# Kernel optimization log

Measured on AMD Instinct MI355X. Metric: run time of the kernel, lower is better.

## Reference

```python
import jax, jax.numpy as jnp
import numpy as np

B, N, IN, H, L, C = 2048, 100, 64, 256, 3, 3
NEG_SLOPE = 0.2


def setup_inputs() -> dict:
    key = jax.random.key(0)
    ks = jax.random.split(key, 11)
    s = lambda k, sh: jax.random.normal(k, sh, dtype=jnp.float32) * 0.05
    return {
        'x': jax.random.normal(ks[0], (B, N, IN), dtype=jnp.float32),
        'W_exp': s(ks[1], (IN, H)), 'b_exp': s(ks[2], (H,)),
        'W_l': s(ks[3], (L, H, H)), 'b_l': s(ks[4], (L, H)),
        'W_r': s(ks[5], (L, H, H)), 'b_r': s(ks[6], (L, H)),
        'att': s(ks[7], (L, H)), 'bias': s(ks[8], (L, H)),
        'W_fc': s(ks[9], (H, C)), 'b_fc': s(ks[10], (C,)),
    }


def _make_pe(n, d):
    pos = jnp.arange(n, dtype=jnp.float32)[:, None]
    div = jnp.exp(jnp.arange(0, d, 2, dtype=jnp.float32) * (-jnp.log(jnp.float32(10000.0)) / d))
    pe = jnp.zeros((n, d), dtype=jnp.float32)
    pe = pe.at[:, 0::2].set(jnp.sin(pos * div))
    pe = pe.at[:, 1::2].set(jnp.cos(pos * div))
    return pe


def _edges(n):
    # bidirectional chain + self loops (GATv2Conv add_self_loops=True)
    src = np.concatenate([np.arange(n - 1), np.arange(1, n), np.arange(n)])
    dst = np.concatenate([np.arange(1, n), np.arange(n - 1), np.arange(n)])
    return jnp.asarray(src), jnp.asarray(dst)


def _gatv2_conv(x, src, dst, Wl, bl, Wr, br, a, b, n):
    # x: [B,N,H]; PyG GATv2Conv, heads=1, share_weights=False
    xl = x @ Wl + bl                      # source transform [B,N,H]
    xr = x @ Wr + br                      # target transform [B,N,H]
    m = jax.nn.leaky_relu(xl[:, src] + xr[:, dst], NEG_SLOPE)   # [B,E,H]
    logits = jnp.einsum('beh,h->be', m, a)                      # [B,E]
    seg_max = jax.vmap(lambda l: jax.ops.segment_max(l, dst, num_segments=n))(logits)
    ex = jnp.exp(logits - seg_max[:, dst])
    denom = jax.vmap(lambda e: jax.ops.segment_sum(e, dst, num_segments=n))(ex)
    alpha = ex / denom[:, dst]                                  # [B,E]
    msgs = alpha[:, :, None] * xl[:, src]                       # [B,E,H]
    out = jax.vmap(lambda mm: jax.ops.segment_sum(mm, dst, num_segments=n))(msgs)
    return out + b


def reference(x, W_exp, b_exp, W_l, b_l, W_r, b_r, att, bias, W_fc, b_fc):
    n = x.shape[1]
    src, dst = _edges(n)
    x0 = x @ W_exp + b_exp + _make_pe(n, W_exp.shape[1])   # expander + positional encoding
    # Faithful to original: the loop feeds batch.x (= x0) into every conv layer,
    # so the output of the loop is the LAST conv applied to x0.
    h = x0
    for l in range(W_l.shape[0]):
        h = _gatv2_conv(x0, src, dst, W_l[l], b_l[l], W_r[l], b_r[l], att[l], bias[l], n)
    pooled = h.sum(axis=1)                                 # global_add_pool -> [B,H]
    return pooled @ W_fc + b_fc                            # [B,num_classes]
```

## Files before the change

kernel.cpp:

```cpp
#include <hip/hip_runtime.h>
#include <hip/hip_bf16.h>
#include <hip/hip_fp16.h>

#define BB 2048
#define NN 100
#define INF_ 64
#define HH 256
#define CC 3
#define HP 136

typedef __attribute__((ext_vector_type(8))) _Float16 h8v;
typedef __attribute__((ext_vector_type(2))) _Float16 h2v;
typedef __attribute__((ext_vector_type(2))) __fp16   g2v;
typedef __attribute__((ext_vector_type(4))) float f4v;

static __device__ __forceinline__ unsigned int pkh(float lo, float hi) {
    union { g2v g; unsigned int u; } c;
    c.g = __builtin_amdgcn_cvt_pkrtz(lo, hi);
    return c.u;
}

__global__ __launch_bounds__(256) void precompute_k(
    const float* __restrict__ W_exp, const float* __restrict__ b_exp,
    const float* __restrict__ W_l, const float* __restrict__ b_l,
    const float* __restrict__ W_r, const float* __restrict__ b_r,
    float* __restrict__ Wcomb, float* __restrict__ cadd)
{
    int r = blockIdx.x;
    int z = blockIdx.y;
    int t = threadIdx.x;
    const float* Wg = (z ? W_r : W_l) + 2 * HH * HH;
    const float* bg = (z ? b_r : b_l) + 2 * HH;

    __shared__ float sa[HH];
    float a;
    if (r < INF_) {
        a = W_exp[r * HH + t];
    } else {
        int n = r - INF_;
        float div = expf((float)(t & 254) * (-0.03597789207803f));
        float ang = (float)n * div;
        a = b_exp[t] + ((t & 1) ? cosf(ang) : sinf(ang));
    }
    sa[t] = a;
    __syncthreads();

    float acc = 0.f;
    #pragma unroll 8
    for (int h = 0; h < HH; ++h)
        acc += sa[h] * Wg[h * HH + t];

    if (r < INF_) Wcomb[(z * INF_ + r) * HH + t] = acc;
    else          cadd[(z * NN + (r - INF_)) * HH + t] = acc + bg[t];
}

#define N_WF 32768
#define N_CF4 14336

__global__ __launch_bounds__(256) void rearrange_k(
    const float* __restrict__ Wcomb, const float* __restrict__ cadd,
    unsigned short* __restrict__ WF, float* __restrict__ CFf)
{
    int i = blockIdx.x * 256 + threadIdx.x;
    if (i < N_WF) {
        int j = i & 7, lane = (i >> 3) & 63, ks = (i >> 9) & 1;
        int nt = (i >> 10) & 15, z = (i >> 14) & 1;
        int k = ks * 32 + 4 * (lane >> 4) + (j & 3) + 16 * (j >> 2);
        int n = nt * 16 + (lane & 15);
        __half h = __float2half(Wcomb[(z * INF_ + k) * HH + n]);
        WF[i] = __half_as_ushort(h);
    } else if (i < N_WF + N_CF4) {
        int i2 = i - N_WF;
        int lane = i2 & 63, nt = (i2 >> 6) & 15;
        int zm = i2 >> 10;
        int mt = zm % 7, z = zm / 7;
        int node = mt * 16 + (lane & 15);
        int feat = nt * 16 + (lane >> 4) * 4;
        float4 v = {0.f, 0.f, 0.f, 0.f};
        if (node < NN)
            v = *(const float4*)&cadd[(z * NN + node) * HH + feat];
        *(float4*)&CFf[(size_t)i2 * 4] = v;
    }
}

__global__ __launch_bounds__(512, 4) void fused_k(
    const float* __restrict__ x,
    const unsigned short* __restrict__ WF, const float* __restrict__ CFf,
    const float* __restrict__ Wcomb, const float* __restrict__ cadd,
    const float* __restrict__ att, const float* __restrict__ bias,
    const float* __restrict__ Wfc, const float* __restrict__ bfc,
    float* __restrict__ out)
{
    __shared__ unsigned short sxl[NN * HP];
    __shared__ unsigned short sxr[NN * HP];
    __shared__ unsigned short sxs[896 * 8];
    __shared__ unsigned int satt2[HH / 2];

    int b = blockIdx.x, t = threadIdx.x;
    int wave = t >> 6, lane = t & 63, g = lane >> 4, li = lane & 15;

    if (t < HH / 2) satt2[t] = pkh(att[2 * HH + 2 * t], att[2 * HH + 2 * t + 1]);

    const float* xb = x + (size_t)b * (NN * INF_);
    for (int s = t; s < 896; s += 512) {
        int sl = s & 63, ks = (s >> 6) & 1, mt = s >> 7;
        int m = mt * 16 + (sl & 15), gg = sl >> 4;
        union { h8v v; unsigned int u[4]; } a;
        if (m < NN) {
            float4 u = *(const float4*)&xb[m * INF_ + ks * 32 + 4 * gg];
            float4 v = *(const float4*)&xb[m * INF_ + ks * 32 + 16 + 4 * gg];
            a.u[0] = pkh(u.x, u.y);
            a.u[1] = pkh(u.z, u.w);
            a.u[2] = pkh(v.x, v.y);
            a.u[3] = pkh(v.z, v.w);
        } else {
            a.u[0] = a.u[1] = a.u[2] = a.u[3] = 0u;
        }
        *(h8v*)&sxs[s * 8] = a.v;
    }

    int q8 = t >> 3, c8 = (t & 7) * 8;
    int eBL[5], eBR[5];
    bool eva[5];
    float pv[5], pa[5];
    #pragma unroll
    for (int i = 0; i < 5; ++i) {
        int e = q8 + 64 * i;
        bool inr = (e < 300);
        int es = inr ? (e / 3) : 0;
        int ed = es + (e - 3 * es) - 1;
        bool v = inr && ed >= 0 && ed < NN;
        eva[i] = v;
        int dd = v ? ed : 0;
        eBL[i] = 2 * (es * HP + c8);
        eBR[i] = 2 * (dd * HP + c8);
        pv[i] = 0.f; pa[i] = 0.f;
    }

    int z = wave >> 2;
    int w4 = wave & 3;
    __syncthreads();

    const h8v* WFp = (const h8v*)WF;
    const f4v* CF4 = (const f4v*)CFf;
    const h8v* sp  = (const h8v*)sxs;

    #pragma unroll
    for (int h = 0; h < 2; ++h) {
        int nt0 = h * 8 + w4 * 2;
        h8v w00 = WFp[((z * 16 + nt0) * 2 + 0) * 64 + lane];
        h8v w01 = WFp[((z * 16 + nt0) * 2 + 1) * 64 + lane];
        h8v w10 = WFp[((z * 16 + nt0 + 1) * 2 + 0) * 64 + lane];
        h8v w11 = WFp[((z * 16 + nt0 + 1) * 2 + 1) * 64 + lane];
        unsigned short* dstp = z ? sxr : sxl;
        int colbase = w4 * 32 + g * 4;
        #pragma unroll
        for (int mt = 0; mt < 7; ++mt) {
            h8v a0 = sp[mt * 128 + lane];
            h8v a1 = sp[mt * 128 + 64 + lane];
            int node = mt * 16 + li;
            bool wr = (mt < 6 || li < 4);
            int el = node * HP + colbase;

            f4v c0 = CF4[((z * 7 + mt) * 16 + nt0) * 64 + lane];
            c0 = __builtin_amdgcn_mfma_f32_16x16x32_f16(w00, a0, c0, 0, 0, 0);
            c0 = __builtin_amdgcn_mfma_f32_16x16x32_f16(w01, a1, c0, 0, 0, 0);
            if (wr) {
                uint2 v0 = { pkh(c0[0], c0[1]), pkh(c0[2], c0[3]) };
                *(uint2*)&dstp[el] = v0;
            }
            f4v c1 = CF4[((z * 7 + mt) * 16 + nt0 + 1) * 64 + lane];
            c1 = __builtin_amdgcn_mfma_f32_16x16x32_f16(w10, a0, c1, 0, 0, 0);
            c1 = __builtin_amdgcn_mfma_f32_16x16x32_f16(w11, a1, c1, 0, 0, 0);
            if (wr) {
                uint2 v1 = { pkh(c1[0], c1[1]), pkh(c1[2], c1[3]) };
                *(uint2*)&dstp[el + 16] = v1;
            }
        }
        __syncthreads();

        #pragma unroll
        for (int cc = 0; cc < 2; ++cc) {
            uint4 atv = *(const uint4*)&satt2[h * 64 + cc * 32 + (t & 7) * 4];
            int cb = cc * 128;
            #pragma unroll
            for (int i = 0; i < 5; ++i) {
                if (eva[i]) {
                    uint4 ua = *(const uint4*)((const char*)sxl + (eBL[i] + cb));
                    uint4 ub = *(const uint4*)((const char*)sxr + (eBR[i] + cb));
                    float fv = 0.f, fa = 0.f;
                    #define PROC(UA, UB, AT) { \
                        union UU { unsigned int u; h2v h; g2v g; }; \
                        UU xa, xb2, vv, va, at; \
                        xa.u = (UA); xb2.u = (UB); at.u = (AT); \
                        vv.h = xa.h + xb2.h;               \
                        va.u = vv.u & 0x7FFF7FFFu;         \
                        fv = __builtin_amdgcn_fdot2(at.g, vv.g, fv, false); \
                        fa = __builtin_amdgcn_fdot2(at.g, va.g, fa, false); }
                    PROC(ua.x, ub.x, atv.x);
                    PROC(ua.y, ub.y, atv.y);
                    PROC(ua.z, ub.z, atv.z);
                    PROC(ua.w, ub.w, atv.w);
                    #undef PROC
                    pv[i] += fv; pa[i] += fa;
                }
            }
        }
        __syncthreads();
    }

    float* lg      = (float*)sxs;
    float* wvp     = lg + 304;
    float* partial = wvp + 104;
    float* ypart   = partial + 16;

    #pragma unroll
    for (int i = 0; i < 5; ++i) {
        float s = fmaf(0.6f, pv[i], 0.4f * pa[i]);
        s += __shfl_xor(s, 1, 64);
        s += __shfl_xor(s, 2, 64);
        s += __shfl_xor(s, 4, 64);
        int e = q8 + 64 * i;
        if ((t & 7) == 0 && e < 300)
            lg[e] = eva[i] ? s : -1e30f;
    }
    __syncthreads();

    if (t < NN) {
        int i = t;
        float w = 0.f;
        #pragma unroll
        for (int dj = -1; dj <= 1; ++dj) {
            int j = i + dj;
            if (j < 0 || j >= NN) continue;
            float l0 = (j - 1 >= 0) ? lg[3 * (j - 1) + 2] : -1e30f;
            float l1 = lg[3 * j + 1];
            float l2 = (j + 1 < NN) ? lg[3 * (j + 1) + 0] : -1e30f;
            float mx = fmaxf(fmaxf(l0, l1), l2);
            float den = expf(l0 - mx) + expf(l1 - mx) + expf(l2 - mx);
            float myl = lg[3 * i + dj + 1];
            w += expf(myl - mx) / den;
        }
        wvp[i] = w;
    }
    __syncthreads();

    {
        int r0 = wave * 13;
        int r1 = (r0 + 13 < NN) ? r0 + 13 : NN;
        float acc = 0.f;
        for (int i = r0; i < r1; ++i)
            acc = fmaf(wvp[i], xb[i * INF_ + lane], acc);
        ypart[wave * 64 + lane] = acc;
    }
    __syncthreads();
    if (t < 64) {
        float s = 0.f;
        #pragma unroll
        for (int w = 0; w < 8; ++w) s += ypart[w * 64 + t];
        ypart[t] = s;
    }
    __syncthreads();

    if (t < HH) {
        float p = 100.f * bias[2 * HH + t];
        #pragma unroll
        for (int k = 0; k < INF_; k += 4) {
            float4 y4 = *(const float4*)&ypart[k];
            p = fmaf(y4.x, Wcomb[(k + 0) * HH + t], p);
            p = fmaf(y4.y, Wcomb[(k + 1) * HH + t], p);
            p = fmaf(y4.z, Wcomb[(k + 2) * HH + t], p);
            p = fmaf(y4.w, Wcomb[(k + 3) * HH + t], p);
        }
        #pragma unroll
        for (int i = 0; i < NN; i += 4) {
            float4 w4v = *(const float4*)&wvp[i];
            p = fmaf(w4v.x, cadd[(i + 0) * HH + t], p);
            p = fmaf(w4v.y, cadd[(i + 1) * HH + t], p);
            p = fmaf(w4v.z, cadd[(i + 2) * HH + t], p);
            p = fmaf(w4v.w, cadd[(i + 3) * HH + t], p);
        }

        float p0 = p * Wfc[t * 3 + 0];
        float p1 = p * Wfc[t * 3 + 1];
        float p2 = p * Wfc[t * 3 + 2];
        #pragma unroll
        for (int off = 32; off; off >>= 1) {
            p0 += __shfl_down(p0, off, 64);
            p1 += __shfl_down(p1, off, 64);
            p2 += __shfl_down(p2, off, 64);
        }
        if (lane == 0) {
            partial[wave * 3 + 0] = p0;
            partial[wave * 3 + 1] = p1;
            partial[wave * 3 + 2] = p2;
        }
    }
    __syncthreads();
    if (t < CC) {
        out[(size_t)b * CC + t] =
            partial[0 * 3 + t] + partial[1 * 3 + t] +
            partial[2 * 3 + t] + partial[3 * 3 + t] + bfc[t];
    }
}

extern "C" void kernel_launch(void* const* d_in, const int* in_sizes, int n_in,
                              void* d_out, int out_size, void* d_ws, size_t ws_size,
                              hipStream_t stream) {
    const float* x     = (const float*)d_in[0];
    const float* W_exp = (const float*)d_in[1];
    const float* b_exp = (const float*)d_in[2];
    const float* W_l   = (const float*)d_in[3];
    const float* b_l   = (const float*)d_in[4];
    const float* W_r   = (const float*)d_in[5];
    const float* b_r   = (const float*)d_in[6];
    const float* att   = (const float*)d_in[7];
    const float* bias  = (const float*)d_in[8];
    const float* W_fc  = (const float*)d_in[9];
    const float* b_fc  = (const float*)d_in[10];
    float* out = (float*)d_out;

    char* ws = (char*)d_ws;
    float* Wcomb = (float*)ws;
    float* cadd  = (float*)(ws + 131072);
    unsigned short* WF = (unsigned short*)(ws + 131072 + 204800);
    float* CFf = (float*)(ws + 131072 + 204800 + 65536);

    precompute_k<<<dim3(164, 2), 256, 0, stream>>>(W_exp, b_exp, W_l, b_l, W_r, b_r,
                                                   Wcomb, cadd);
    rearrange_k<<<184, 256, 0, stream>>>(Wcomb, cadd, WF, CFf);
    fused_k<<<BB, 512, 0, stream>>>(x, WF, CFf, Wcomb, cadd, att, bias, W_fc, b_fc, out);
}
```

Measured before the change: 83.97 us.

## Compute attention logits in MFMA registers via lane shuffles instead of LDS staging

The xl/xr projection results are no longer written to shared memory as fp16 and re-read per edge. Each wave now computes both the left and right projections for its feature slice. Chain-neighbour edge terms are formed directly from accumulator registers with lane shuffles, and per-wave partial logits are reduced across waves through a small LDS array. Edges that cross 16-node tile boundaries are recomputed with extra MFMAs, which removes the large LDS buffers and one sync phase. The cost is more MFMA work per wave and a cross-wave reduction.

```diff
diff --git a/kernel.cpp b/kernel.cpp
--- a/kernel.cpp
+++ b/kernel.cpp
@@ -7,10 +7,8 @@
 #define INF_ 64
 #define HH 256
 #define CC 3
-#define HP 136
 
 typedef __attribute__((ext_vector_type(8))) _Float16 h8v;
-typedef __attribute__((ext_vector_type(2))) _Float16 h2v;
 typedef __attribute__((ext_vector_type(2))) __fp16   g2v;
 typedef __attribute__((ext_vector_type(4))) float f4v;
 
@@ -18,6 +16,12 @@
     union { g2v g; unsigned int u; } c;
     c.g = __builtin_amdgcn_cvt_pkrtz(lo, hi);
     return c.u;
+}
+static __device__ __forceinline__ float lane_m1(float v) {
+    return __shfl_up(v, 1, 64);
+}
+static __device__ __forceinline__ float lane_p1(float v) {
+    return __shfl_down(v, 1, 64);
 }
 
 __global__ __launch_bounds__(256) void precompute_k(
@@ -91,15 +95,12 @@
     const float* __restrict__ Wfc, const float* __restrict__ bfc,
     float* __restrict__ out)
 {
-    __shared__ unsigned short sxl[NN * HP];
-    __shared__ unsigned short sxr[NN * HP];
     __shared__ unsigned short sxs[896 * 8];
-    __shared__ unsigned int satt2[HH / 2];
+    __shared__ float spart[8][304];
+    __shared__ float spartB[8][16];
 
     int b = blockIdx.x, t = threadIdx.x;
     int wave = t >> 6, lane = t & 63, g = lane >> 4, li = lane & 15;
-
-    if (t < HH / 2) satt2[t] = pkh(att[2 * HH + 2 * t], att[2 * HH + 2 * t + 1]);
 
     const float* xb = x + (size_t)b * (NN * INF_);
     for (int s = t; s < 896; s += 512) {
@@ -119,110 +120,123 @@
         *(h8v*)&sxs[s * 8] = a.v;
     }
 
-    int q8 = t >> 3, c8 = (t & 7) * 8;
-    int eBL[5], eBR[5];
-    bool eva[5];
-    float pv[5], pa[5];
+    int nt0 = wave * 2;
+    const h8v* WFp = (const h8v*)WF;
+    h8v wf[2][2][2];
     #pragma unroll
-    for (int i = 0; i < 5; ++i) {
-        int e = q8 + 64 * i;
-        bool inr = (e < 300);
-        int es = inr ? (e / 3) : 0;
-        int ed = es + (e - 3 * es) - 1;
-        bool v = inr && ed >= 0 && ed < NN;
-        eva[i] = v;
-        int dd = v ? ed : 0;
-        eBL[i] = 2 * (es * HP + c8);
-        eBR[i] = 2 * (dd * HP + c8);
-        pv[i] = 0.f; pa[i] = 0.f;
-    }
-
-    int z = wave >> 2;
-    int w4 = wave & 3;
-    __syncthreads();
-
-    const h8v* WFp = (const h8v*)WF;
+    for (int j = 0; j < 2; ++j)
+        #pragma unroll
+        for (int z = 0; z < 2; ++z)
+            #pragma unroll
+            for (int ks = 0; ks < 2; ++ks)
+                wf[j][z][ks] = WFp[((z * 16 + nt0 + j) * 2 + ks) * 64 + lane];
+    f4v aA = *(const f4v*)&att[2 * HH + nt0 * 16 + g * 4];
+    f4v aB = *(const f4v*)&att[2 * HH + (nt0 + 1) * 16 + g * 4];
+
+    __syncthreads();
+
+    const h8v* sp = (const h8v*)sxs;
     const f4v* CF4 = (const f4v*)CFf;
-    const h8v* sp  = (const h8v*)sxs;
 
     #pragma unroll
-    for (int h = 0; h < 2; ++h) {
-        int nt0 = h * 8 + w4 * 2;
-        h8v w00 = WFp[((z * 16 + nt0) * 2 + 0) * 64 + lane];
-        h8v w01 = WFp[((z * 16 + nt0) * 2 + 1) * 64 + lane];
-        h8v w10 = WFp[((z * 16 + nt0 + 1) * 2 + 0) * 64 + lane];
-        h8v w11 = WFp[((z * 16 + nt0 + 1) * 2 + 1) * 64 + lane];
-        unsigned short* dstp = z ? sxr : sxl;
-        int colbase = w4 * 32 + g * 4;
-        #pragma unroll
-        for (int mt = 0; mt < 7; ++mt) {
-            h8v a0 = sp[mt * 128 + lane];
-            h8v a1 = sp[mt * 128 + 64 + lane];
-            int node = mt * 16 + li;
-            bool wr = (mt < 6 || li < 4);
-            int el = node * HP + colbase;
-
-            f4v c0 = CF4[((z * 7 + mt) * 16 + nt0) * 64 + lane];
-            c0 = __builtin_amdgcn_mfma_f32_16x16x32_f16(w00, a0, c0, 0, 0, 0);
-            c0 = __builtin_amdgcn_mfma_f32_16x16x32_f16(w01, a1, c0, 0, 0, 0);
-            if (wr) {
-                uint2 v0 = { pkh(c0[0], c0[1]), pkh(c0[2], c0[3]) };
-                *(uint2*)&dstp[el] = v0;
+    for (int mt = 0; mt < 7; ++mt) {
+        h8v a0 = sp[mt * 128 + lane];
+        h8v a1 = sp[mt * 128 + 64 + lane];
+        float sv0 = 0.f, sv1 = 0.f, sv2 = 0.f;
+        float sa0 = 0.f, sa1 = 0.f, sa2 = 0.f;
+        #pragma unroll
+        for (int j = 0; j < 2; ++j) {
+            int nt = nt0 + j;
+            f4v cl = CF4[((0 * 7 + mt) * 16 + nt) * 64 + lane];
+            f4v cr = CF4[((1 * 7 + mt) * 16 + nt) * 64 + lane];
+            cl = __builtin_amdgcn_mfma_f32_16x16x32_f16(wf[j][0][0], a0, cl, 0, 0, 0);
+            cl = __builtin_amdgcn_mfma_f32_16x16x32_f16(wf[j][0][1], a1, cl, 0, 0, 0);
+            cr = __builtin_amdgcn_mfma_f32_16x16x32_f16(wf[j][1][0], a0, cr, 0, 0, 0);
+            cr = __builtin_amdgcn_mfma_f32_16x16x32_f16(wf[j][1][1], a1, cr, 0, 0, 0);
+            f4v at = j ? aB : aA;
+            #pragma unroll
+            for (int r = 0; r < 4; ++r) {
+                float crm = lane_m1(cr[r]);
+                float crp = lane_p1(cr[r]);
+                float v1 = cl[r] + cr[r];
+                float vm = cl[r] + crm;
+                float vp = cl[r] + crp;
+                sv1 = fmaf(at[r], v1, sv1); sa1 = fmaf(at[r], fabsf(v1), sa1);
+                sv0 = fmaf(at[r], vm, sv0); sa0 = fmaf(at[r], fabsf(vm), sa0);
+                sv2 = fmaf(at[r], vp, sv2); sa2 = fmaf(at[r], fabsf(vp), sa2);
             }
-            f4v c1 = CF4[((z * 7 + mt) * 16 + nt0 + 1) * 64 + lane];
-            c1 = __builtin_amdgcn_mfma_f32_16x16x32_f16(w10, a0, c1, 0, 0, 0);
-            c1 = __builtin_amdgcn_mfma_f32_16x16x32_f16(w11, a1, c1, 0, 0, 0);
-            if (wr) {
-                uint2 v1 = { pkh(c1[0], c1[1]), pkh(c1[2], c1[3]) };
-                *(uint2*)&dstp[el + 16] = v1;
+        }
+        float r0v = fmaf(0.6f, sv0, 0.4f * sa0);
+        float r1v = fmaf(0.6f, sv1, 0.4f * sa1);
+        float r2v = fmaf(0.6f, sv2, 0.4f * sa2);
+        r0v += __shfl_xor(r0v, 16, 64); r0v += __shfl_xor(r0v, 32, 64);
+        r1v += __shfl_xor(r1v, 16, 64); r1v += __shfl_xor(r1v, 32, 64);
+        r2v += __shfl_xor(r2v, 16, 64); r2v += __shfl_xor(r2v, 32, 64);
+        int node = mt * 16 + li;
+        if (lane < 16 && node < NN) {
+            float* row = &spart[wave][3 * node];
+            if (li > 0)  row[0] = r0v;
+            row[1] = r1v;
+            if (li < 15) row[2] = r2v;
+        }
+    }
+
+    {
+        int c = li;
+        int s, d;
+        if (c < 6)       { s = 16 * (c + 1) - 1; d = s + 1; }
+        else if (c < 12) { s = 16 * (c - 5);     d = s - 1; }
+        else             { s = 0; d = 0; }
+        int slS = (s >> 4) * 128 + g * 16 + (s & 15);
+        int slD = (d >> 4) * 128 + g * 16 + (d & 15);
+        h8v e0 = sp[slS], e1 = sp[slS + 64];
+        h8v e2 = sp[slD], e3 = sp[slD + 64];
+        float sv = 0.f, sa = 0.f;
+        #pragma unroll
+        for (int j = 0; j < 2; ++j) {
+            int feat = (nt0 + j) * 16 + g * 4;
+            float4 ca = *(const float4*)&cadd[(0 * NN + s) * HH + feat];
+            float4 cb = *(const float4*)&cadd[(1 * NN + d) * HH + feat];
+            f4v c0;
+            c0[0] = ca.x + cb.x; c0[1] = ca.y + cb.y;
+            c0[2] = ca.z + cb.z; c0[3] = ca.w + cb.w;
+            c0 = __builtin_amdgcn_mfma_f32_16x16x32_f16(wf[j][0][0], e0, c0, 0, 0, 0);
+            c0 = __builtin_amdgcn_mfma_f32_16x16x32_f16(wf[j][0][1], e1, c0, 0, 0, 0);
+            c0 = __builtin_amdgcn_mfma_f32_16x16x32_f16(wf[j][1][0], e2, c0, 0, 0, 0);
+            c0 = __builtin_amdgcn_mfma_f32_16x16x32_f16(wf[j][1][1], e3, c0, 0, 0, 0);
+            f4v at = j ? aB : aA;
+            #pragma unroll
+            for (int r = 0; r < 4; ++r) {
+                sv = fmaf(at[r], c0[r], sv);
+                sa = fmaf(at[r], fabsf(c0[r]), sa);
             }
         }
-        __syncthreads();
-
-        #pragma unroll
-        for (int cc = 0; cc < 2; ++cc) {
-            uint4 atv = *(const uint4*)&satt2[h * 64 + cc * 32 + (t & 7) * 4];
-            int cb = cc * 128;
-            #pragma unroll
-            for (int i = 0; i < 5; ++i) {
-                if (eva[i]) {
-                    uint4 ua = *(const uint4*)((const char*)sxl + (eBL[i] + cb));
-                    uint4 ub = *(const uint4*)((const char*)sxr + (eBR[i] + cb));
-                    float fv = 0.f, fa = 0.f;
-                    #define PROC(UA, UB, AT) { \
-                        union UU { unsigned int u; h2v h; g2v g; }; \
-                        UU xa, xb2, vv, va, at; \
-                        xa.u = (UA); xb2.u = (UB); at.u = (AT); \
-                        vv.h = xa.h + xb2.h;               \
-                        va.u = vv.u & 0x7FFF7FFFu;         \
-                        fv = __builtin_amdgcn_fdot2(at.g, vv.g, fv, false); \
-                        fa = __builtin_amdgcn_fdot2(at.g, va.g, fa, false); }
-                    PROC(ua.x, ub.x, atv.x);
-                    PROC(ua.y, ub.y, atv.y);
-                    PROC(ua.z, ub.z, atv.z);
-                    PROC(ua.w, ub.w, atv.w);
-                    #undef PROC
-                    pv[i] += fv; pa[i] += fa;
-                }
-            }
-        }
-        __syncthreads();
-    }
+        float sb = fmaf(0.6f, sv, 0.4f * sa);
+        sb += __shfl_xor(sb, 16, 64);
+        sb += __shfl_xor(sb, 32, 64);
+        if (lane < 16) spartB[wave][lane] = sb;
+    }
+    __syncthreads();
 
     float* lg      = (float*)sxs;
     float* wvp     = lg + 304;
-    float* partial = wvp + 104;
+    float* partial = wvp + 108;
     float* ypart   = partial + 16;
 
-    #pragma unroll
-    for (int i = 0; i < 5; ++i) {
-        float s = fmaf(0.6f, pv[i], 0.4f * pa[i]);
-        s += __shfl_xor(s, 1, 64);
-        s += __shfl_xor(s, 2, 64);
-        s += __shfl_xor(s, 4, 64);
-        int e = q8 + 64 * i;
-        if ((t & 7) == 0 && e < 300)
-            lg[e] = eva[i] ? s : -1e30f;
+    if (t < 300) {
+        int q3 = t % 3, s = t / 3;
+        int slot = -1;
+        if (q3 == 2 && (s & 15) == 15)               slot = s >> 4;
+        else if (q3 == 0 && t > 0 && (s & 15) == 0)  slot = 5 + (s >> 4);
+        float v = 0.f;
+        if (slot >= 0) {
+            #pragma unroll
+            for (int w = 0; w < 8; ++w) v += spartB[w][slot];
+        } else {
+            #pragma unroll
+            for (int w = 0; w < 8; ++w) v += spart[w][t];
+        }
+        lg[t] = v;
     }
     __syncthreads();
 
```

Result: slower. 88.16 us (+5.0%).
